# Performance work log

Measured on AMD Instinct MI355X. Metric: run time of the kernel, lower is better.

## Reference

```python
import jax, jax.numpy as jnp
import numpy as np
import math

B, S, D, H = 2, 2048, 1024, 16
HD = D // H  # head_dims = 64


def setup_inputs() -> dict:
    key = jax.random.key(0)
    ks = jax.random.split(key, 8)
    sc = 1.0 / math.sqrt(D)
    return {
        "queries": jax.random.normal(ks[0], (B, S, D), jnp.float32),
        "keys":    jax.random.normal(ks[1], (B, S, D), jnp.float32),
        "values":  jax.random.normal(ks[2], (B, S, D), jnp.float32),
        # causal mask: 1 where attending allowed, 0 where blocked (masked_fill on ==0)
        "mask": jnp.tril(jnp.ones((S, S), jnp.int32)),
        "Wq": jax.random.normal(ks[3], (D, D), jnp.float32) * sc,
        "bq": jnp.zeros((D,), jnp.float32),
        "Wk": jax.random.normal(ks[4], (D, D), jnp.float32) * sc,
        "bk": jnp.zeros((D,), jnp.float32),
        "Wv": jax.random.normal(ks[5], (D, D), jnp.float32) * sc,
        "bv": jnp.zeros((D,), jnp.float32),
        "Wo": jax.random.normal(ks[6], (D, D), jnp.float32) * sc,
        "bo": jnp.zeros((D,), jnp.float32),
    }


def _split_heads(x):
    # (B, S, D) -> (B, H, S, HD)
    return x.reshape(B, S, H, HD).transpose(0, 2, 1, 3)


def reference(queries, keys, values, mask, Wq, bq, Wk, bk, Wv, bv, Wo, bo):
    q = queries @ Wq + bq
    k = keys @ Wk + bk
    # NOTE: faithful to source quirk — V is projected from the ALREADY-PROJECTED keys
    # (original: keys = self.W_keys(keys); values = self.W_values(keys))
    v = k @ Wv + bv
    q, k, v = _split_heads(q), _split_heads(k), _split_heads(v)
    # naive full NxN attention, as in the source
    scores = jnp.einsum("bhqd,bhkd->bhqk", q, k) / math.sqrt(HD)
    scores = jnp.where(mask == 0, jnp.float32(-1e9), scores)
    probs = jax.nn.softmax(scores, axis=-1)
    attn = jnp.einsum("bhqk,bhkd->bhqd", probs, v)
    attn = attn.transpose(0, 2, 1, 3).reshape(B, S, D)
    return attn @ Wo + bo
```

## Files before the change

### kernel.cpp

```cpp
#include <hip/hip_runtime.h>

typedef unsigned short u16;
typedef unsigned int u32;
typedef __bf16 bf16x8 __attribute__((ext_vector_type(8)));
typedef float f32x4 __attribute__((ext_vector_type(4)));
typedef float f32x16 __attribute__((ext_vector_type(16)));
typedef unsigned int u32x4v __attribute__((ext_vector_type(4)));

#define MFMA16(a, b, c) __builtin_amdgcn_mfma_f32_16x16x32_bf16(a, b, c, 0, 0, 0)
#define MFMA32(a, b, c) __builtin_amdgcn_mfma_f32_32x32x16_bf16(a, b, c, 0, 0, 0)

__device__ __forceinline__ void gload16(const void* g, void* l) {
  __builtin_amdgcn_global_load_lds((const __attribute__((address_space(1))) void*)g,
                                   (__attribute__((address_space(3))) void*)l, 16, 0, 0);
}

__device__ __forceinline__ u16 f2bf(float f) {
  u32 u = __builtin_bit_cast(u32, f);
  u += 0x7fffu + ((u >> 16) & 1u);
  return (u16)(u >> 16);
}
__device__ __forceinline__ u32 pack2(float a, float b) {
  u32 r;
  asm("v_cvt_pk_bf16_f32 %0, %1, %2" : "=v"(r) : "v"(a), "v"(b));
  return r;
}

__global__ __launch_bounds__(256) void cvt_kernel(const float* __restrict__ q,
                                                  const float* __restrict__ k,
                                                  u16* __restrict__ qb,
                                                  u16* __restrict__ kb) {
  const float* src = blockIdx.y ? k : q;
  u16* dst = blockIdx.y ? kb : qb;
  size_t i = (size_t)blockIdx.x * 256 + threadIdx.x;
  float4 v = ((const float4*)src)[i];
  uint2 o;
  o.x = pack2(v.x, v.y);
  o.y = pack2(v.z, v.w);
  ((uint2*)dst)[i] = o;
}

__global__ __launch_bounds__(256) void wtrans_kernel(const float* W0, const float* W1,
                                                     const float* W2, const float* W3,
                                                     u16* T0, u16* T1, u16* T2, u16* T3) {
  int z = blockIdx.z;
  const float* W = z == 0 ? W0 : z == 1 ? W1 : z == 2 ? W2 : W3;
  u16* T = z == 0 ? T0 : z == 1 ? T1 : z == 2 ? T2 : T3;
  __shared__ float tile[64][65];
  int tr = blockIdx.y * 64, tc = blockIdx.x * 64;
  int tid = threadIdx.x;
  int c4 = (tid & 15) * 4, r0 = tid >> 4;
#pragma unroll
  for (int i = 0; i < 4; i++) {
    int r = r0 + i * 16;
    float4 v = *(const float4*)(W + (size_t)(tr + r) * 1024 + tc + c4);
    tile[r][c4 + 0] = v.x; tile[r][c4 + 1] = v.y;
    tile[r][c4 + 2] = v.z; tile[r][c4 + 3] = v.w;
  }
  __syncthreads();
#pragma unroll
  for (int i = 0; i < 2; i++) {
    int c = tid + i * 256;
    int n = c >> 3, kg = c & 7;
    uint4 o;
    o.x = pack2(tile[kg * 8 + 0][n], tile[kg * 8 + 1][n]);
    o.y = pack2(tile[kg * 8 + 2][n], tile[kg * 8 + 3][n]);
    o.z = pack2(tile[kg * 8 + 4][n], tile[kg * 8 + 5][n]);
    o.w = pack2(tile[kg * 8 + 6][n], tile[kg * 8 + 7][n]);
    *(uint4*)(T + (size_t)(tc + n) * 1024 + tr + kg * 8) = o;
  }
}

template <int MODE>
__global__ __launch_bounds__(256) void gemm_kernel(
    const u16* A0, const u16* B0, const float* bias0, void* C0, float scale0,
    const u16* A1, const u16* B1, const float* bias1, void* C1, float scale1,
    int M, int N, int K) {
  const u16* A = A0; const u16* Bt = B0; const float* bias = bias0; void* Cout = C0;
  float scale = scale0;
  if (blockIdx.z) { A = A1; Bt = B1; bias = bias1; Cout = C1; scale = scale1; }

  __shared__ __attribute__((aligned(16))) char sAB[49152];
  const int tid = threadIdx.x, lane = tid & 63, w = tid >> 6;
  const int l15 = lane & 15, quad = lane >> 4;
  const int wm = (w >> 1) * 64, wn = (w & 1) * 32;
  const int m0 = blockIdx.y * 128, n0 = blockIdx.x * 64;

  const int lrow = lane >> 3, lcg = (lane & 7) ^ lrow;
  const u16* aP[4]; const u16* bP[2];
#pragma unroll
  for (int i = 0; i < 4; i++)
    aP[i] = A + (size_t)(m0 + w * 32 + i * 8 + lrow) * K + lcg * 8;
#pragma unroll
  for (int i = 0; i < 2; i++)
    bP[i] = Bt + (size_t)(n0 + w * 16 + i * 8 + lrow) * K + lcg * 8;

  int aoff[4], boff[2];
#pragma unroll
  for (int t = 0; t < 4; t++) {
    int ra = wm + t * 16 + l15;
    aoff[t] = ra * 128 + ((quad ^ (ra & 7)) * 16);
  }
#pragma unroll
  for (int t = 0; t < 2; t++) {
    int rb = wn + t * 16 + l15;
    boff[t] = 16384 + rb * 128 + ((quad ^ (rb & 7)) * 16);
  }

#pragma unroll
  for (int i = 0; i < 4; i++) { gload16(aP[i], sAB + w * 4096 + i * 1024); aP[i] += 64; }
#pragma unroll
  for (int i = 0; i < 2; i++) { gload16(bP[i], sAB + 16384 + w * 2048 + i * 1024); bP[i] += 64; }

  f32x4 acc[4][2] = {};
  int cur = 0;
  for (int k = 0; k < K; k += 64) {
    __syncthreads();
    if (k + 64 < K) {
      char* dst = sAB + (cur ^ 1) * 24576;
#pragma unroll
      for (int i = 0; i < 4; i++) { gload16(aP[i], dst + w * 4096 + i * 1024); aP[i] += 64; }
#pragma unroll
      for (int i = 0; i < 2; i++) { gload16(bP[i], dst + 16384 + w * 2048 + i * 1024); bP[i] += 64; }
    }
    const char* buf = sAB + cur * 24576;
#pragma unroll
    for (int kt = 0; kt < 2; kt++) {
      bf16x8 af[4], bfr[2];
#pragma unroll
      for (int t = 0; t < 4; t++) af[t] = *(const bf16x8*)(buf + (aoff[t] ^ (kt * 64)));
#pragma unroll
      for (int t = 0; t < 2; t++) bfr[t] = *(const bf16x8*)(buf + (boff[t] ^ (kt * 64)));
#pragma unroll
      for (int mt = 0; mt < 4; mt++)
#pragma unroll
        for (int nt = 0; nt < 2; nt++)
          acc[mt][nt] = MFMA16(af[mt], bfr[nt], acc[mt][nt]);
    }
    cur ^= 1;
  }

#pragma unroll
  for (int nt = 0; nt < 2; nt++) {
    int col = n0 + wn + nt * 16 + l15;
    float bv = bias[col];
#pragma unroll
    for (int mt = 0; mt < 4; mt++) {
      int row = m0 + wm + mt * 16 + quad * 4;
      if (MODE == 0) {
        u16* C = (u16*)Cout;
#pragma unroll
        for (int r = 0; r < 4; r++)
          C[(size_t)(row + r) * N + col] = f2bf((acc[mt][nt][r] + bv) * scale);
      } else if (MODE == 1) {
        u16* C = (u16*)Cout;
        int hh = col >> 6, hd = col & 63;
        int bb = row >> 11, s = row & 2047;
        uint2 o;
        o.x = pack2((acc[mt][nt][0] + bv) * scale, (acc[mt][nt][1] + bv) * scale);
        o.y = pack2((acc[mt][nt][2] + bv) * scale, (acc[mt][nt][3] + bv) * scale);
        *(uint2*)(C + ((size_t)((bb * 16 + hh) * 64 + hd) * 2048 + s)) = o;
      } else {
        float* C = (float*)Cout;
#pragma unroll
        for (int r = 0; r < 4; r++)
          C[(size_t)(row + r) * N + col] = (acc[mt][nt][r] + bv) * scale;
      }
    }
  }
}

__global__ __launch_bounds__(256, 2) void attn_kernel(const u16* __restrict__ qw,
                                                      const u16* __restrict__ kw,
                                                      const u16* __restrict__ vw,
                                                      u16* __restrict__ aout) {
  __shared__ __attribute__((aligned(16))) char sKV[4][16384];
  const int bh = blockIdx.x, p = blockIdx.y;
  const int b = bh >> 4, h = bh & 15;
  const int tid = threadIdx.x, lane = tid & 63, w = tid >> 6;
  const int g = w & 1, qh = w >> 1;
  const int c = lane & 31, hi = lane >> 5;
  const int qcol = qh * 32 + c;
  const int lrow = lane >> 3, lcg = (lane & 7) ^ lrow;
  const u16* kb0 = kw + (size_t)(b * 2048) * 1024 + h * 64;
  const u16* vb0 = vw + (size_t)bh * 64 * 2048;

  int kvoff[2][4];
#pragma unroll
  for (int m = 0; m < 2; m++)
#pragma unroll
    for (int kt = 0; kt < 4; kt++) {
      int row = m * 32 + c;
      kvoff[m][kt] = row * 128 + (((kt * 2 + hi) ^ (row & 7)) * 16);
    }

  auto stage = [&](int j, int slot) {
    char* dst = sKV[slot];
#pragma unroll
    for (int i = 0; i < 2; i++) {
      int rr = w * 16 + i * 8 + lrow;
      gload16(kb0 + (size_t)(j * 64 + rr) * 1024 + lcg * 8, dst + w * 2048 + i * 1024);
      gload16(vb0 + (size_t)rr * 2048 + j * 64 + lcg * 8, dst + 8192 + w * 2048 + i * 1024);
    }
  };

  for (int phase = 0; phase < 2; ++phase) {
    const int t = phase ? (31 - p) : p;
    __syncthreads();

    bf16x8 qf[4];
    {
      const u16* qbase =
          qw + (size_t)(b * 2048 + t * 64 + qcol) * 1024 + h * 64 + hi * 8;
#pragma unroll
      for (int kt = 0; kt < 4; kt++) qf[kt] = *(const bf16x8*)(qbase + kt * 16);
    }
    stage(0, 0);
    if (t >= 1) stage(1, 1);

    f32x16 o0 = {}, o1 = {};
    float lsum = 0.f;
    const int R = (t + 2) >> 1;
    for (int r = 0; r < R; ++r) {
      __syncthreads();
      if (2 * r + 2 <= t) stage(2 * r + 2, (2 * r + 2) & 3);
      if (2 * r + 3 <= t) stage(2 * r + 3, (2 * r + 3) & 3);
      const int jg = 2 * r + g;
      if (jg <= t) {
        const char* buf = sKV[jg & 3];
        f32x16 S0 = {}, S1 = {};
        __builtin_amdgcn_s_setprio(1);
#pragma unroll
        for (int kt = 0; kt < 4; kt++) {
          bf16x8 k0 = *(const bf16x8*)(buf + kvoff[0][kt]);
          bf16x8 k1 = *(const bf16x8*)(buf + kvoff[1][kt]);
          S0 = MFMA32(k0, qf[kt], S0);
          S1 = MFMA32(k1, qf[kt], S1);
        }
        __builtin_amdgcn_s_setprio(0);
        const bool diag = (jg == t);
        u32 pw0[8], pw1[8];
        auto epack = [&](const f32x16& S, int mbase, u32* pw) {
          float e[16];
#pragma unroll
          for (int rg = 0; rg < 16; rg++) {
            float ev = __builtin_amdgcn_exp2f(S[rg]);
            if (diag) {
              int row = mbase + (rg & 3) + 8 * (rg >> 2) + 4 * hi;
              if (row > qcol) ev = 0.f;
            }
            e[rg] = ev;
          }
          float s = 0.f;
#pragma unroll
          for (int rg = 0; rg < 16; rg += 4)
            s += (e[rg] + e[rg + 1]) + (e[rg + 2] + e[rg + 3]);
          lsum += s;
#pragma unroll
          for (int i = 0; i < 8; i++) pw[i] = pack2(e[2 * i], e[2 * i + 1]);
        };
        epack(S0, 0, pw0);
        epack(S1, 32, pw1);
        __builtin_amdgcn_s_setprio(1);
#pragma unroll
        for (int kt2 = 0; kt2 < 4; kt2++) {
          const u32* pws = (kt2 < 2) ? pw0 : pw1;
          const int bb = (kt2 & 1) * 4;
          auto s0 = __builtin_amdgcn_permlane32_swap(pws[bb + 0], pws[bb + 2], false, false);
          auto s1 = __builtin_amdgcn_permlane32_swap(pws[bb + 1], pws[bb + 3], false, false);
          u32x4v pq = {s0[0], s1[0], s0[1], s1[1]};
          bf16x8 pf = __builtin_bit_cast(bf16x8, pq);
          bf16x8 v0 = *(const bf16x8*)(buf + 8192 + kvoff[0][kt2]);
          bf16x8 v1 = *(const bf16x8*)(buf + 8192 + kvoff[1][kt2]);
          o0 = MFMA32(v0, pf, o0);
          o1 = MFMA32(v1, pf, o1);
        }
        __builtin_amdgcn_s_setprio(0);
      }
    }

    __syncthreads();
    if (g == 1) {
      float* red = (float*)(sKV[0] + qh * 8448);
      float* redl = (float*)(sKV[0] + qh * 8448 + 8192);
#pragma unroll
      for (int rg = 0; rg < 16; rg++) {
        red[lane * 32 + rg] = o0[rg];
        red[lane * 32 + 16 + rg] = o1[rg];
      }
      redl[lane] = lsum;
    }
    __syncthreads();
    if (g == 0) {
      const float* red = (const float*)(sKV[0] + qh * 8448);
      const float* redl = (const float*)(sKV[0] + qh * 8448 + 8192);
#pragma unroll
      for (int rg = 0; rg < 16; rg++) {
        o0[rg] += red[lane * 32 + rg];
        o1[rg] += red[lane * 32 + 16 + rg];
      }
      lsum += redl[lane];
      lsum += __shfl_xor(lsum, 32, 64);
      float inv = 1.0f / lsum;
      int token = b * 2048 + t * 64 + qcol;
      u16* outp = aout + (size_t)token * 1024 + h * 64;
#pragma unroll
      for (int i = 0; i < 4; i++) {
        uint2 ov;
        ov.x = pack2(o0[4 * i + 0] * inv, o0[4 * i + 1] * inv);
        ov.y = pack2(o0[4 * i + 2] * inv, o0[4 * i + 3] * inv);
        *(uint2*)(outp + i * 8 + hi * 4) = ov;
        ov.x = pack2(o1[4 * i + 0] * inv, o1[4 * i + 1] * inv);
        ov.y = pack2(o1[4 * i + 2] * inv, o1[4 * i + 3] * inv);
        *(uint2*)(outp + 32 + i * 8 + hi * 4) = ov;
      }
    }
  }
}

extern "C" void kernel_launch(void* const* d_in, const int* in_sizes, int n_in,
                              void* d_out, int out_size, void* d_ws, size_t ws_size,
                              hipStream_t stream) {
  const float* queries = (const float*)d_in[0];
  const float* keys    = (const float*)d_in[1];
  const float* Wq = (const float*)d_in[4];
  const float* bq = (const float*)d_in[5];
  const float* Wk = (const float*)d_in[6];
  const float* bk = (const float*)d_in[7];
  const float* Wv = (const float*)d_in[8];
  const float* bv = (const float*)d_in[9];
  const float* Wo = (const float*)d_in[10];
  const float* bo = (const float*)d_in[11];

  char* ws = (char*)d_ws;
  u16* qb  = (u16*)(ws);
  u16* kb  = (u16*)(ws + (8u << 20));
  u16* qP  = (u16*)(ws + (16u << 20));
  u16* kP  = (u16*)(ws);
  u16* vP  = (u16*)(ws + (8u << 20));
  u16* WqT = (u16*)(ws + (24u << 20));
  u16* WkT = (u16*)(ws + (26u << 20));
  u16* WvT = (u16*)(ws + (28u << 20));
  u16* WoT = (u16*)(ws + (30u << 20));

  const float kscale = 1.4426950408889634f / 8.0f;

  cvt_kernel<<<dim3(4096, 2), 256, 0, stream>>>(queries, keys, qb, kb);
  wtrans_kernel<<<dim3(16, 16, 4), 256, 0, stream>>>(Wq, Wk, Wv, Wo, WqT, WkT, WvT, WoT);
  gemm_kernel<0><<<dim3(16, 32, 2), 256, 0, stream>>>(
      qb, WqT, bq, qP, kscale, kb, WkT, bk, kP, 1.0f, 4096, 1024, 1024);
  gemm_kernel<1><<<dim3(16, 32, 1), 256, 0, stream>>>(
      kP, WvT, bv, vP, 1.0f, kP, WvT, bv, vP, 1.0f, 4096, 1024, 1024);
  attn_kernel<<<dim3(32, 16), 256, 0, stream>>>(qP, kP, vP, qP);
  gemm_kernel<2><<<dim3(16, 32, 1), 256, 0, stream>>>(
      qP, WoT, bo, d_out, 1.0f, qP, WoT, bo, d_out, 1.0f, 4096, 1024, 1024);
}
```

Before: 215.7 us.

## Repartition attention warps to split keys instead of queries, reducing K LDS reads

Each warp now owns 32 keys of a 64-key tile and computes scores for all 64 queries, so one K fragment load feeds two MFMAs. Each warp's PV step covers its own 32-key slice for all 64 queries and both halves of head_dim. Before, every warp reloaded the full K tile. The epilogue becomes a four-way cross-warp reduction through LDS, and every warp now writes output, where before half the warps did. The change trades fewer K LDS reads for more Q registers, four accumulators instead of two, and a heavier final reduction.

```diff
diff --git a/kernel.cpp b/kernel.cpp
--- a/kernel.cpp
+++ b/kernel.cpp
@@ -175,24 +175,31 @@
                                                       const u16* __restrict__ vw,
                                                       u16* __restrict__ aout) {
   __shared__ __attribute__((aligned(16))) char sKV[4][16384];
+  __shared__ float slq[4][64];
+  char* sflat = (char*)sKV;
   const int bh = blockIdx.x, p = blockIdx.y;
   const int b = bh >> 4, h = bh & 15;
   const int tid = threadIdx.x, lane = tid & 63, w = tid >> 6;
-  const int g = w & 1, qh = w >> 1;
+  const int g = w & 1, kh = w >> 1;
   const int c = lane & 31, hi = lane >> 5;
-  const int qcol = qh * 32 + c;
   const int lrow = lane >> 3, lcg = (lane & 7) ^ lrow;
   const u16* kb0 = kw + (size_t)(b * 2048) * 1024 + h * 64;
   const u16* vb0 = vw + (size_t)bh * 64 * 2048;
 
-  int kvoff[2][4];
-#pragma unroll
-  for (int m = 0; m < 2; m++)
-#pragma unroll
-    for (int kt = 0; kt < 4; kt++) {
-      int row = m * 32 + c;
-      kvoff[m][kt] = row * 128 + (((kt * 2 + hi) ^ (row & 7)) * 16);
-    }
+  int koffK[4], koffV[2][2];
+  {
+    int krow = kh * 32 + c;
+#pragma unroll
+    for (int kt = 0; kt < 4; kt++)
+      koffK[kt] = krow * 128 + (((kt * 2 + hi) ^ (krow & 7)) * 16);
+#pragma unroll
+    for (int m = 0; m < 2; m++) {
+      int vrow = m * 32 + c;
+#pragma unroll
+      for (int kt2 = 0; kt2 < 2; kt2++)
+        koffV[m][kt2] = 8192 + vrow * 128 + ((((kh * 2 + kt2) * 2 + hi) ^ (vrow & 7)) * 16);
+    }
+  }
 
   auto stage = [&](int j, int slot) {
     char* dst = sKV[slot];
@@ -208,18 +215,19 @@
     const int t = phase ? (31 - p) : p;
     __syncthreads();
 
-    bf16x8 qf[4];
-    {
+    bf16x8 qf[2][4];
+#pragma unroll
+    for (int qb2 = 0; qb2 < 2; qb2++) {
       const u16* qbase =
-          qw + (size_t)(b * 2048 + t * 64 + qcol) * 1024 + h * 64 + hi * 8;
-#pragma unroll
-      for (int kt = 0; kt < 4; kt++) qf[kt] = *(const bf16x8*)(qbase + kt * 16);
+          qw + (size_t)(b * 2048 + t * 64 + qb2 * 32 + c) * 1024 + h * 64 + hi * 8;
+#pragma unroll
+      for (int kt = 0; kt < 4; kt++) qf[qb2][kt] = *(const bf16x8*)(qbase + kt * 16);
     }
     stage(0, 0);
     if (t >= 1) stage(1, 1);
 
-    f32x16 o0 = {}, o1 = {};
-    float lsum = 0.f;
+    f32x16 o00 = {}, o01 = {}, o10 = {}, o11 = {};
+    float ls0 = 0.f, ls1 = 0.f;
     const int R = (t + 2) >> 1;
     for (int r = 0; r < R; ++r) {
       __syncthreads();
@@ -232,22 +240,21 @@
         __builtin_amdgcn_s_setprio(1);
 #pragma unroll
         for (int kt = 0; kt < 4; kt++) {
-          bf16x8 k0 = *(const bf16x8*)(buf + kvoff[0][kt]);
-          bf16x8 k1 = *(const bf16x8*)(buf + kvoff[1][kt]);
-          S0 = MFMA32(k0, qf[kt], S0);
-          S1 = MFMA32(k1, qf[kt], S1);
+          bf16x8 kf = *(const bf16x8*)(buf + koffK[kt]);
+          S0 = MFMA32(kf, qf[0][kt], S0);
+          S1 = MFMA32(kf, qf[1][kt], S1);
         }
         __builtin_amdgcn_s_setprio(0);
         const bool diag = (jg == t);
         u32 pw0[8], pw1[8];
-        auto epack = [&](const f32x16& S, int mbase, u32* pw) {
+        auto epack = [&](const f32x16& S, int qc, u32* pw, float& ls) {
           float e[16];
 #pragma unroll
           for (int rg = 0; rg < 16; rg++) {
             float ev = __builtin_amdgcn_exp2f(S[rg]);
             if (diag) {
-              int row = mbase + (rg & 3) + 8 * (rg >> 2) + 4 * hi;
-              if (row > qcol) ev = 0.f;
+              int row = kh * 32 + (rg & 3) + 8 * (rg >> 2) + 4 * hi;
+              if (row > qc) ev = 0.f;
             }
             e[rg] = ev;
           }
@@ -255,64 +262,72 @@
 #pragma unroll
           for (int rg = 0; rg < 16; rg += 4)
             s += (e[rg] + e[rg + 1]) + (e[rg + 2] + e[rg + 3]);
-          lsum += s;
+          ls += s;
 #pragma unroll
           for (int i = 0; i < 8; i++) pw[i] = pack2(e[2 * i], e[2 * i + 1]);
         };
-        epack(S0, 0, pw0);
-        epack(S1, 32, pw1);
+        epack(S0, c, pw0, ls0);
+        epack(S1, 32 + c, pw1, ls1);
         __builtin_amdgcn_s_setprio(1);
 #pragma unroll
-        for (int kt2 = 0; kt2 < 4; kt2++) {
-          const u32* pws = (kt2 < 2) ? pw0 : pw1;
-          const int bb = (kt2 & 1) * 4;
-          auto s0 = __builtin_amdgcn_permlane32_swap(pws[bb + 0], pws[bb + 2], false, false);
-          auto s1 = __builtin_amdgcn_permlane32_swap(pws[bb + 1], pws[bb + 3], false, false);
-          u32x4v pq = {s0[0], s1[0], s0[1], s1[1]};
-          bf16x8 pf = __builtin_bit_cast(bf16x8, pq);
-          bf16x8 v0 = *(const bf16x8*)(buf + 8192 + kvoff[0][kt2]);
-          bf16x8 v1 = *(const bf16x8*)(buf + 8192 + kvoff[1][kt2]);
-          o0 = MFMA32(v0, pf, o0);
-          o1 = MFMA32(v1, pf, o1);
+        for (int kt2 = 0; kt2 < 2; kt2++) {
+          const int bb = kt2 * 4;
+          auto a0 = __builtin_amdgcn_permlane32_swap(pw0[bb + 0], pw0[bb + 2], false, false);
+          auto a1 = __builtin_amdgcn_permlane32_swap(pw0[bb + 1], pw0[bb + 3], false, false);
+          u32x4v pq0 = {a0[0], a1[0], a0[1], a1[1]};
+          bf16x8 pf0 = __builtin_bit_cast(bf16x8, pq0);
+          auto b0 = __builtin_amdgcn_permlane32_swap(pw1[bb + 0], pw1[bb + 2], false, false);
+          auto b1 = __builtin_amdgcn_permlane32_swap(pw1[bb + 1], pw1[bb + 3], false, false);
+          u32x4v pq1 = {b0[0], b1[0], b0[1], b1[1]};
+          bf16x8 pf1 = __builtin_bit_cast(bf16x8, pq1);
+          bf16x8 v0 = *(const bf16x8*)(buf + koffV[0][kt2]);
+          bf16x8 v1 = *(const bf16x8*)(buf + koffV[1][kt2]);
+          o00 = MFMA32(v0, pf0, o00);
+          o10 = MFMA32(v1, pf0, o10);
+          o01 = MFMA32(v0, pf1, o01);
+          o11 = MFMA32(v1, pf1, o11);
         }
         __builtin_amdgcn_s_setprio(0);
       }
     }
 
+    ls0 += __shfl_xor(ls0, 32, 64);
+    ls1 += __shfl_xor(ls1, 32, 64);
     __syncthreads();
-    if (g == 1) {
-      float* red = (float*)(sKV[0] + qh * 8448);
-      float* redl = (float*)(sKV[0] + qh * 8448 + 8192);
-#pragma unroll
-      for (int rg = 0; rg < 16; rg++) {
-        red[lane * 32 + rg] = o0[rg];
-        red[lane * 32 + 16 + rg] = o1[rg];
-      }
-      redl[lane] = lsum;
+    {
+      char* myr = sflat + w * 16384;
+      auto putq = [&](int qid, const f32x16& v) {
+#pragma unroll
+        for (int ch = 0; ch < 4; ch++) {
+          f32x4 x = {v[ch * 4 + 0], v[ch * 4 + 1], v[ch * 4 + 2], v[ch * 4 + 3]};
+          *(f32x4*)(myr + (qid * 4 + ch) * 1024 + lane * 16) = x;
+        }
+      };
+      putq(0, o00); putq(1, o01); putq(2, o10); putq(3, o11);
+      slq[w][hi * 32 + c] = hi ? ls1 : ls0;
     }
     __syncthreads();
-    if (g == 0) {
-      const float* red = (const float*)(sKV[0] + qh * 8448);
-      const float* redl = (const float*)(sKV[0] + qh * 8448 + 8192);
-#pragma unroll
-      for (int rg = 0; rg < 16; rg++) {
-        o0[rg] += red[lane * 32 + rg];
-        o1[rg] += red[lane * 32 + 16 + rg];
-      }
-      lsum += redl[lane];
-      lsum += __shfl_xor(lsum, 32, 64);
-      float inv = 1.0f / lsum;
-      int token = b * 2048 + t * 64 + qcol;
-      u16* outp = aout + (size_t)token * 1024 + h * 64;
+    {
+      f32x16 acc = {};
+#pragma unroll
+      for (int wv = 0; wv < 4; wv++)
+#pragma unroll
+        for (int ch = 0; ch < 4; ch++) {
+          f32x4 rr = *(const f32x4*)(sflat + wv * 16384 + (w * 4 + ch) * 1024 + lane * 16);
+          acc[ch * 4 + 0] += rr[0]; acc[ch * 4 + 1] += rr[1];
+          acc[ch * 4 + 2] += rr[2]; acc[ch * 4 + 3] += rr[3];
+        }
+      const int q = (w & 1) * 32 + c;
+      float lt = ((slq[0][q] + slq[1][q]) + (slq[2][q] + slq[3][q]));
+      float inv = 1.0f / lt;
+      int token = b * 2048 + t * 64 + q;
+      u16* outp = aout + (size_t)token * 1024 + h * 64 + (w >> 1) * 32;
 #pragma unroll
       for (int i = 0; i < 4; i++) {
         uint2 ov;
-        ov.x = pack2(o0[4 * i + 0] * inv, o0[4 * i + 1] * inv);
-        ov.y = pack2(o0[4 * i + 2] * inv, o0[4 * i + 3] * inv);
+        ov.x = pack2(acc[4 * i + 0] * inv, acc[4 * i + 1] * inv);
+        ov.y = pack2(acc[4 * i + 2] * inv, acc[4 * i + 3] * inv);
         *(uint2*)(outp + i * 8 + hi * 4) = ov;
-        ov.x = pack2(o1[4 * i + 0] * inv, o1[4 * i + 1] * inv);
-        ov.y = pack2(o1[4 * i + 2] * inv, o1[4 * i + 3] * inv);
-        *(uint2*)(outp + 32 + i * 8 + hi * 4) = ov;
       }
     }
   }
```

Result: no change. 215.4 us (-0.1%).
